# Performance work log

Hardware: AMD Instinct MI355X
Metric: run time of the kernel (lower is better)

The kernel has to match this reference:

```python
import jax, jax.numpy as jnp
import numpy as np

DIM = 192
NUM_HEADS = 6
WH, WW = 7, 7
N = WH * WW  # 49 tokens per window
C2 = 2 * DIM  # concatenated channel dim = 384
SCALE = (DIM // NUM_HEADS) ** -0.5  # module uses dim//num_heads, not C2//num_heads
NW = 64  # number of windows per image
B_ = 2048  # num_windows * batch


def _relative_position_index():
    ch = np.arange(WH)
    cw = np.arange(WW)
    coords = np.stack(np.meshgrid(ch, cw, indexing='ij')).reshape(2, -1)  # [2, N]
    rel = coords[:, :, None] - coords[:, None, :]  # [2, N, N]
    rel = rel.transpose(1, 2, 0).astype(np.int64)  # [N, N, 2]
    rel[..., 0] += WH - 1
    rel[..., 1] += WW - 1
    rel[..., 0] *= 2 * WW - 1
    return jnp.asarray(rel.sum(-1))  # [N, N]

REL_IDX = _relative_position_index()


def setup_inputs() -> dict:
    key = jax.random.key(0)
    ks = jax.random.split(key, 8)
    x = jax.random.normal(ks[0], (B_, N, DIM), dtype=jnp.float32)
    y = jax.random.normal(ks[1], (B_, N, DIM), dtype=jnp.float32)
    mask = jax.random.normal(ks[2], (NW, N, N), dtype=jnp.float32)
    w_qkv = jax.random.normal(ks[3], (6 * DIM, C2), dtype=jnp.float32) * 0.02
    b_qkv = jnp.zeros((6 * DIM,), dtype=jnp.float32)
    w_proj = jax.random.normal(ks[4], (DIM, C2), dtype=jnp.float32) * 0.02
    b_proj = jnp.zeros((DIM,), dtype=jnp.float32)
    bias_table = jax.random.normal(ks[5], ((2 * WH - 1) * (2 * WW - 1), NUM_HEADS), dtype=jnp.float32) * 0.02
    return {"x": x, "y": y, "mask": mask, "w_qkv": w_qkv, "b_qkv": b_qkv,
            "w_proj": w_proj, "b_proj": b_proj, "bias_table": bias_table}


def reference(x, y, mask, w_qkv, b_qkv, w_proj, b_proj, bias_table):
    Bc = x.shape[0]
    Dh = C2 // NUM_HEADS  # 64
    xy = jnp.concatenate([x, y], axis=2)  # [B_, N, 2*dim]
    qkv = xy @ w_qkv.T + b_qkv  # [B_, N, 6*dim]
    qkv = qkv.reshape(Bc, N, 3, NUM_HEADS, Dh).transpose(2, 0, 3, 1, 4)  # [3, B_, H, N, Dh]
    q, k, v = qkv[0] * SCALE, qkv[1], qkv[2]
    attn = jnp.einsum('bhnd,bhmd->bhnm', q, k)  # [B_, H, N, N]
    rpb = bias_table[REL_IDX]  # [N, N, H]
    attn = attn + rpb.transpose(2, 0, 1)[None]
    nW = mask.shape[0]
    attn = attn.reshape(Bc // nW, nW, NUM_HEADS, N, N) + mask[None, :, None]
    attn = attn.reshape(Bc, NUM_HEADS, N, N)
    attn = jax.nn.softmax(attn, axis=-1)
    out = jnp.einsum('bhnm,bhmd->bhnd', attn, v)  # [B_, H, N, Dh]
    out = out.transpose(0, 2, 1, 3).reshape(Bc, N, C2)
    return out @ w_proj.T + b_proj  # [B_, N, dim]
```

## Files before the change

### kernel.cpp

```cpp
#include <hip/hip_runtime.h>
#include <hip/hip_bf16.h>


typedef __attribute__((ext_vector_type(8))) short short8;
typedef __attribute__((ext_vector_type(4))) float f32x4;

#define SCALE 0.17677669529663687f

#define WQF_OFF    0ul
#define WQF_BYTES  (864ul*1024)
#define WPF_OFF    (WQF_OFF + WQF_BYTES)
#define WPF_BYTES  (144ul*1024)
#define COMB_OFF   (WPF_OFF + WPF_BYTES)
#define COMB_BYTES (64ul*6*4096*4)
#define XYF_OFF    (COMB_OFF + COMB_BYTES)
#define XYF_BYTES  (2048ul*48*1024)
#define OF_OFF     (XYF_OFF + XYF_BYTES)
#define OF_BYTES   XYF_BYTES
#define WS_NEED    (OF_OFF + OF_BYTES)

__device__ __forceinline__ unsigned short f2bf(float f){
  unsigned u = __builtin_bit_cast(unsigned, f);
  u = u + 0x7fffu + ((u >> 16) & 1u);
  return (unsigned short)(u >> 16);
}
__device__ __forceinline__ unsigned long long pack4(float4 v){
  return (unsigned long long)f2bf(v.x) | ((unsigned long long)f2bf(v.y) << 16)
       | ((unsigned long long)f2bf(v.z) << 32) | ((unsigned long long)f2bf(v.w) << 48);
}

__global__ void k0_wfrag(const float* __restrict__ wq_f, const float* __restrict__ wp_f,
                         unsigned short* __restrict__ wqf, unsigned short* __restrict__ wpf){
  int t = blockIdx.x*256 + threadIdx.x;
  int fragidx = t >> 6, l = t & 63;
  const float* src; unsigned short* dst;
  if (fragidx < 864){
    int h = fragidx/144, rem = fragidx - h*144;
    int ct = rem/12, kt = rem - ct*12;
    int row = (ct>>2)*384 + h*64 + (ct&3)*16 + (l&15);
    src = wq_f + (long)row*384 + kt*32 + (l>>4)*8;
    dst = wqf + (long)fragidx*512 + l*8;
  } else {
    int fid = fragidx - 864;
    int ct = fid/12, kt = fid - ct*12;
    int row = ct*16 + (l&15);
    src = wp_f + (long)row*384 + kt*32 + (l>>4)*8;
    dst = wpf + (long)fid*512 + l*8;
  }
  short8 v;
  #pragma unroll
  for (int e = 0; e < 8; ++e) v[e] = (short)f2bf(src[e]);
  *(short8*)dst = v;
}

__global__ void prep_comb(const float* __restrict__ mask, const float* __restrict__ btab,
                          float* __restrict__ comb){
  int idx = blockIdx.x * 256 + threadIdx.x;
  int j = idx & 63, i = (idx >> 6) & 63, rest = idx >> 12;
  int h = rest % 6, w = rest / 6;
  float v;
  if (i < 49 && j < 49){
    int di = i / 7 - j / 7 + 6;
    int dj = i % 7 - j % 7 + 6;
    v = btab[(di * 13 + dj) * 6 + h] + mask[(w * 49 + i) * 49 + j];
  } else {
    v = (j >= 49) ? -1e30f : 0.0f;
  }
  comb[idx] = v;
}

__global__ void k1_xyfrag(const float* __restrict__ x, const float* __restrict__ y,
                          unsigned short* __restrict__ xyf){
  const int kt  = blockIdx.x;
  const int win = blockIdx.y;
  const int mt  = threadIdx.x >> 6;
  const int l   = threadIdx.x & 63;
  const int row = mt*16 + (l & 15);
  const int c0  = kt*32 + (l >> 4)*8;
  short8 v = {};
  if (row < 49){
    const float* src = (kt < 6) ? (x + ((long)win*49 + row)*192 + c0)
                                : (y + ((long)win*49 + row)*192 + (c0 - 192));
    float4 f0 = *(const float4*)src, f1 = *(const float4*)(src+4);
    unsigned long long lo = pack4(f0), hi = pack4(f1);
    #pragma unroll
    for (int e = 0; e < 4; ++e){ v[e] = (short)(lo >> (16*e)); v[4+e] = (short)(hi >> (16*e)); }
  }
  *(short8*)(xyf + (((long)win*12 + kt)*4 + mt)*512 + l*8) = v;
}

__device__ __forceinline__ int swz(int r, int b){ return b ^ ((r & 7) << 4); }
__device__ __forceinline__ int a_q (int r, int c){ return 0     + swz(r, r*128 + c*2); }
__device__ __forceinline__ int a_k (int r, int c){ return 8192  + swz(r, r*128 + c*2); }
__device__ __forceinline__ int a_vt(int r, int c){ return 16384 + swz(r, r*128 + c*2); }

__global__ __launch_bounds__(256, 4)
void k2_qkv_attn(const unsigned short* __restrict__ xyf, const unsigned short* __restrict__ wqf,
                 const float* __restrict__ bqkv, const float* __restrict__ comb,
                 unsigned short* __restrict__ Of){
  __shared__ __align__(16) unsigned char smem[24576];
  const int h = blockIdx.x, win = blockIdx.y;
  const int tid = threadIdx.x, w = tid>>6, l = tid&63, l15 = l&15, lg = l>>4;

  float bias[3];
  #pragma unroll
  for (int nt = 0; nt < 3; ++nt){
    int n = w*48 + nt*16 + l15;
    bias[nt] = bqkv[(n>>6)*384 + h*64 + (n&63)];
  }

  f32x4 acc[4][3] = {};
  const unsigned short* Ab = xyf + (long)win*24576;
  const unsigned short* Bb = wqf + ((long)h*12 + w*3)*12*512;
  short8 aA[2][4], bB[2][3];
  #pragma unroll
  for (int mt = 0; mt < 4; ++mt) aA[0][mt] = *(const short8*)(Ab + mt*512 + l*8);
  #pragma unroll
  for (int nt = 0; nt < 3; ++nt) bB[0][nt] = *(const short8*)(Bb + (nt*12)*512 + l*8);
  #pragma unroll
  for (int kt = 0; kt < 12; ++kt){
    const int cur = kt & 1, nxt = cur ^ 1;
    if (kt < 11){
      #pragma unroll
      for (int mt = 0; mt < 4; ++mt)
        aA[nxt][mt] = *(const short8*)(Ab + ((kt+1)*4 + mt)*512 + l*8);
      #pragma unroll
      for (int nt = 0; nt < 3; ++nt)
        bB[nxt][nt] = *(const short8*)(Bb + (nt*12 + kt+1)*512 + l*8);
    }
    #pragma unroll
    for (int nt = 0; nt < 3; ++nt){
      #pragma unroll
      for (int mt = 0; mt < 4; ++mt)
        acc[mt][nt] = __builtin_amdgcn_mfma_f32_16x16x32_bf16(aA[cur][mt], bB[cur][nt], acc[mt][nt], 0, 0, 0);
    }
  }

  const float* cb = comb + ((long)((win & 63)*6 + h))*4096 + (w*16 + l15)*64 + lg*4;
  float4 cbv[4];
  #pragma unroll
  for (int nt = 0; nt < 4; ++nt) cbv[nt] = *(const float4*)(cb + nt*16);

  #pragma unroll
  for (int nt = 0; nt < 3; ++nt){
    int ct = w*3 + nt, s = ct >> 2, d16 = (ct & 3) * 16;
    if (s == 2){
      #pragma unroll
      for (int mt = 0; mt < 4; ++mt){
        float4 vv;
        vv.x = acc[mt][nt][0] + bias[nt]; vv.y = acc[mt][nt][1] + bias[nt];
        vv.z = acc[mt][nt][2] + bias[nt]; vv.w = acc[mt][nt][3] + bias[nt];
        *(unsigned long long*)(smem + a_vt(d16 + l15, mt*16 + lg*4)) = pack4(vv);
      }
    } else {
      float sc = (s == 0) ? SCALE : 1.0f;
      #pragma unroll
      for (int mt = 0; mt < 4; ++mt){
        #pragma unroll
        for (int j = 0; j < 4; ++j){
          int row = mt*16 + lg*4 + j;
          float v = (acc[mt][nt][j] + bias[nt]) * sc;
          int addr = (s == 0) ? a_q(row, d16 + l15) : a_k(row, d16 + l15);
          *(unsigned short*)(smem + addr) = f2bf(v);
        }
      }
    }
  }
  __syncthreads();

  short8 bq[2];
  #pragma unroll
  for (int ks = 0; ks < 2; ++ks)
    bq[ks] = *(const short8*)(smem + a_q(w*16 + l15, ks*32 + lg*8));
  f32x4 st[4] = {};
  #pragma unroll
  for (int ks = 0; ks < 2; ++ks){
    #pragma unroll
    for (int nt = 0; nt < 4; ++nt){
      short8 ak = *(const short8*)(smem + a_k(nt*16 + l15, ks*32 + lg*8));
      st[nt] = __builtin_amdgcn_mfma_f32_16x16x32_bf16(ak, bq[ks], st[nt], 0, 0, 0);
    }
  }
  #pragma unroll
  for (int nt = 0; nt < 4; ++nt){
    st[nt][0] += cbv[nt].x; st[nt][1] += cbv[nt].y;
    st[nt][2] += cbv[nt].z; st[nt][3] += cbv[nt].w;
  }
  float mx;
  {
    float m0 = fmaxf(fmaxf(st[0][0], st[0][1]), fmaxf(st[0][2], st[0][3]));
    float m1 = fmaxf(fmaxf(st[1][0], st[1][1]), fmaxf(st[1][2], st[1][3]));
    float m2 = fmaxf(fmaxf(st[2][0], st[2][1]), fmaxf(st[2][2], st[2][3]));
    float m3 = fmaxf(fmaxf(st[3][0], st[3][1]), fmaxf(st[3][2], st[3][3]));
    mx = fmaxf(fmaxf(m0, m1), fmaxf(m2, m3));
  }
  mx = fmaxf(mx, __shfl_xor(mx, 16));
  mx = fmaxf(mx, __shfl_xor(mx, 32));
  float ssum = 0.f;
  #pragma unroll
  for (int nt = 0; nt < 4; ++nt){
    #pragma unroll
    for (int j = 0; j < 4; ++j){
      float e = __expf(st[nt][j] - mx);
      st[nt][j] = e; ssum += e;
    }
  }
  ssum += __shfl_xor(ssum, 16);
  ssum += __shfl_xor(ssum, 32);
  const float inv = 1.0f / ssum;

  #pragma unroll
  for (int nt = 0; nt < 4; ++nt){
    float4 vv;
    vv.x = st[nt][0]*inv; vv.y = st[nt][1]*inv; vv.z = st[nt][2]*inv; vv.w = st[nt][3]*inv;
    *(unsigned long long*)(smem + a_q(w*16 + l15, nt*16 + lg*4)) = pack4(vv);
  }

  short8 ap[2];
  #pragma unroll
  for (int ks = 0; ks < 2; ++ks)
    ap[ks] = *(const short8*)(smem + a_q(w*16 + l15, ks*32 + lg*8));
  f32x4 oacc[4] = {};
  #pragma unroll
  for (int ks = 0; ks < 2; ++ks){
    #pragma unroll
    for (int nt = 0; nt < 4; ++nt){
      short8 bv = *(const short8*)(smem + a_vt(nt*16 + l15, ks*32 + lg*8));
      oacc[nt] = __builtin_amdgcn_mfma_f32_16x16x32_bf16(ap[ks], bv, oacc[nt], 0, 0, 0);
    }
  }
  #pragma unroll
  for (int nt = 0; nt < 4; ++nt){
    #pragma unroll
    for (int j = 0; j < 4; ++j)
      *(unsigned short*)(smem + a_q(w*16 + lg*4 + j, nt*16 + l15)) = f2bf(oacc[nt][j]);
  }
  unsigned short* Ob = Of + (((long)win*12 + h*2)*4 + w)*512 + l*8;
  #pragma unroll
  for (int ks = 0; ks < 2; ++ks){
    short8 o8 = *(const short8*)(smem + a_q(w*16 + l15, ks*32 + lg*8));
    *(short8*)(Ob + ks*4*512) = o8;
  }
}

__global__ __launch_bounds__(256, 4)
void k3_proj(const unsigned short* __restrict__ Of, const unsigned short* __restrict__ wpf,
             const float* __restrict__ bproj, float* __restrict__ out){
  const int win = blockIdx.x;
  const int tid = threadIdx.x, w = tid>>6, l = tid&63, l15 = l&15, lg = l>>4;
  float bp[3]; int np[3];
  #pragma unroll
  for (int nt = 0; nt < 3; ++nt){
    np[nt] = w*48 + nt*16 + l15;
    bp[nt] = bproj[np[nt]];
  }
  f32x4 acc[4][3] = {};
  const unsigned short* Ab = Of + (long)win*24576;
  const unsigned short* Bb = wpf + (long)(w*3)*12*512;
  short8 aA[2][4], bB[2][3];
  #pragma unroll
  for (int mt = 0; mt < 4; ++mt) aA[0][mt] = *(const short8*)(Ab + mt*512 + l*8);
  #pragma unroll
  for (int nt = 0; nt < 3; ++nt) bB[0][nt] = *(const short8*)(Bb + (nt*12)*512 + l*8);
  #pragma unroll
  for (int kt = 0; kt < 12; ++kt){
    const int cur = kt & 1, nxt = cur ^ 1;
    if (kt < 11){
      #pragma unroll
      for (int mt = 0; mt < 4; ++mt)
        aA[nxt][mt] = *(const short8*)(Ab + ((kt+1)*4 + mt)*512 + l*8);
      #pragma unroll
      for (int nt = 0; nt < 3; ++nt)
        bB[nxt][nt] = *(const short8*)(Bb + (nt*12 + kt+1)*512 + l*8);
    }
    #pragma unroll
    for (int nt = 0; nt < 3; ++nt){
      #pragma unroll
      for (int mt = 0; mt < 4; ++mt)
        acc[mt][nt] = __builtin_amdgcn_mfma_f32_16x16x32_bf16(aA[cur][mt], bB[cur][nt], acc[mt][nt], 0, 0, 0);
    }
  }
  #pragma unroll
  for (int mt = 0; mt < 4; ++mt){
    #pragma unroll
    for (int j = 0; j < 4; ++j){
      int row = mt*16 + lg*4 + j;
      if (row < 49){
        float* o = out + ((long)win*49 + row)*192;
        #pragma unroll
        for (int nt = 0; nt < 3; ++nt)
          o[np[nt]] = acc[mt][nt][j] + bp[nt];
      }
    }
  }
}

#define FB_WQ_ELEMS (1152*384)
#define FB_WP_ELEMS (192*384)
#define FB_WP_OFF   (FB_WQ_ELEMS*2)
#define FB_COMB_OFF (FB_WP_OFF + FB_WP_ELEMS*2)

__global__ void prep_weights_fb(const float* __restrict__ wq_f, const float* __restrict__ wp_f,
                                unsigned short* __restrict__ wq, unsigned short* __restrict__ wp){
  int gid = blockIdx.x * 256 + threadIdx.x;
  if (gid < FB_WQ_ELEMS) wq[gid] = f2bf(wq_f[gid]);
  else { int g = gid - FB_WQ_ELEMS; if (g < FB_WP_ELEMS) wp[g] = f2bf(wp_f[g]); }
}
__device__ __forceinline__ int fb_xy(int r, int c){ return 0      + swz(r, r*768 + c*2); }
__device__ __forceinline__ int fb_q (int r, int c){ return 49152  + swz(r, r*128 + c*2); }
__device__ __forceinline__ int fb_k (int r, int c){ return 57344  + swz(r, r*128 + c*2); }
__device__ __forceinline__ int fb_vt(int r, int c){ return 65536  + swz(r, r*128 + c*2); }
__device__ __forceinline__ int fb_p (int r, int c){ return 73728  + swz(r, r*128 + c*2); }

__global__ __launch_bounds__(256, 2)
void fused_attn_fb(const float* __restrict__ x, const float* __restrict__ y,
                   const float* __restrict__ bqkv, const float* __restrict__ bproj,
                   const unsigned short* __restrict__ wq, const unsigned short* __restrict__ wp,
                   const float* __restrict__ comb, float* __restrict__ out){
  __shared__ __align__(16) unsigned char smem[81920];
  const int b = blockIdx.x, tid = threadIdx.x;
  const int w = tid>>6, l = tid&63, l15 = l&15, lg = l>>4;
  {
    const float4* x4 = (const float4*)x + b * 2352;
    const float4* y4 = (const float4*)y + b * 2352;
    for (int idx = tid; idx < 2352; idx += 256){
      int r = idx / 48, c4 = (idx % 48) * 4;
      float4 vx = x4[idx], vy = y4[idx];
      *(unsigned long long*)(smem + fb_xy(r, c4))       = pack4(vx);
      *(unsigned long long*)(smem + fb_xy(r, 192 + c4)) = pack4(vy);
    }
    for (int idx = tid; idx < 1440; idx += 256){
      int r = 49 + idx / 96, c4 = (idx % 96) * 4;
      *(unsigned long long*)(smem + fb_xy(r, c4)) = 0ull;
    }
  }
  __syncthreads();
  const float* cbB = comb + (long)(b & 63) * (6 * 4096);
  f32x4 pacc[4][3] = {};
  int np[3]; float bp[3];
  #pragma unroll
  for (int nt = 0; nt < 3; ++nt){ np[nt] = w*48 + nt*16 + l15; bp[nt] = bproj[np[nt]]; }
  #pragma unroll 1
  for (int h = 0; h < 6; ++h){
    f32x4 acc[4][3] = {};
    int wrow[3]; float bias[3];
    #pragma unroll
    for (int nt = 0; nt < 3; ++nt){
      int n = np[nt];
      wrow[nt] = (n >> 6) * 384 + h * 64 + (n & 63);
      bias[nt] = bqkv[wrow[nt]];
    }
    #pragma unroll 4
    for (int kt = 0; kt < 12; ++kt){
      int k0 = kt * 32;
      short8 a[4];
      #pragma unroll
      for (int mt = 0; mt < 4; ++mt)
        a[mt] = *(const short8*)(smem + fb_xy(mt*16 + l15, k0 + lg*8));
      #pragma unroll
      for (int nt = 0; nt < 3; ++nt){
        short8 bb = *(const short8*)(wq + (long)wrow[nt]*384 + k0 + lg*8);
        #pragma unroll
        for (int mt = 0; mt < 4; ++mt)
          acc[mt][nt] = __builtin_amdgcn_mfma_f32_16x16x32_bf16(a[mt], bb, acc[mt][nt], 0, 0, 0);
      }
    }
    #pragma unroll
    for (int nt = 0; nt < 3; ++nt){
      int n = np[nt], s = n >> 6, d = n & 63;
      #pragma unroll
      for (int mt = 0; mt < 4; ++mt){
        #pragma unroll
        for (int j = 0; j < 4; ++j){
          int row = mt*16 + lg*4 + j;
          float v = acc[mt][nt][j] + bias[nt];
          if (s == 0) v *= SCALE;
          int addr = (s==0) ? fb_q(row,d) : (s==1) ? fb_k(row,d) : fb_vt(d,row);
          *(unsigned short*)(smem + addr) = f2bf(v);
        }
      }
    }
    __syncthreads();
    short8 aq[2];
    #pragma unroll
    for (int ks = 0; ks < 2; ++ks)
      aq[ks] = *(const short8*)(smem + fb_q(w*16 + l15, ks*32 + lg*8));
    f32x4 sacc[4] = {};
    #pragma unroll
    for (int ks = 0; ks < 2; ++ks)
      #pragma unroll
      for (int nt = 0; nt < 4; ++nt){
        short8 bk = *(const short8*)(smem + fb_k(nt*16 + l15, ks*32 + lg*8));
        sacc[nt] = __builtin_amdgcn_mfma_f32_16x16x32_bf16(aq[ks], bk, sacc[nt], 0, 0, 0);
      }
    const float* cb = cbB + h * 4096;
    float rs[4];
    #pragma unroll
    for (int j = 0; j < 4; ++j){
      int r = w*16 + lg*4 + j;
      #pragma unroll
      for (int nt = 0; nt < 4; ++nt) sacc[nt][j] += cb[r*64 + nt*16 + l15];
      float m = fmaxf(fmaxf(sacc[0][j], sacc[1][j]), fmaxf(sacc[2][j], sacc[3][j]));
      #pragma unroll
      for (int dlt = 1; dlt < 16; dlt <<= 1) m = fmaxf(m, __shfl_xor(m, dlt));
      float ssum = 0.f;
      #pragma unroll
      for (int nt = 0; nt < 4; ++nt){
        float e = __expf(sacc[nt][j] - m);
        sacc[nt][j] = e; ssum += e;
      }
      #pragma unroll
      for (int dlt = 1; dlt < 16; dlt <<= 1) ssum += __shfl_xor(ssum, dlt);
      rs[j] = ssum;
      #pragma unroll
      for (int nt = 0; nt < 4; ++nt)
        *(unsigned short*)(smem + fb_p(r, nt*16 + l15)) = f2bf(sacc[nt][j]);
    }
    short8 ap[2];
    #pragma unroll
    for (int ks = 0; ks < 2; ++ks)
      ap[ks] = *(const short8*)(smem + fb_p(w*16 + l15, ks*32 + lg*8));
    f32x4 oacc[4] = {};
    #pragma unroll
    for (int ks = 0; ks < 2; ++ks)
      #pragma unroll
      for (int nt = 0; nt < 4; ++nt){
        short8 bv = *(const short8*)(smem + fb_vt(nt*16 + l15, ks*32 + lg*8));
        oacc[nt] = __builtin_amdgcn_mfma_f32_16x16x32_bf16(ap[ks], bv, oacc[nt], 0, 0, 0);
      }
    float inv[4];
    #pragma unroll
    for (int j = 0; j < 4; ++j) inv[j] = 1.0f / rs[j];
    #pragma unroll
    for (int nt = 0; nt < 4; ++nt)
      #pragma unroll
      for (int j = 0; j < 4; ++j){
        int row = w*16 + lg*4 + j;
        *(unsigned short*)(smem + fb_p(row, nt*16 + l15)) = f2bf(oacc[nt][j] * inv[j]);
      }
    __syncthreads();
    #pragma unroll
    for (int ks = 0; ks < 2; ++ks){
      short8 ao8[4];
      #pragma unroll
      for (int mt = 0; mt < 4; ++mt)
        ao8[mt] = *(const short8*)(smem + fb_p(mt*16 + l15, ks*32 + lg*8));
      #pragma unroll
      for (int nt = 0; nt < 3; ++nt){
        short8 bb = *(const short8*)(wp + (long)np[nt]*384 + h*64 + ks*32 + lg*8);
        #pragma unroll
        for (int mt = 0; mt < 4; ++mt)
          pacc[mt][nt] = __builtin_amdgcn_mfma_f32_16x16x32_bf16(ao8[mt], bb, pacc[mt][nt], 0, 0, 0);
      }
    }
  }
  #pragma unroll
  for (int mt = 0; mt < 4; ++mt)
    #pragma unroll
    for (int j = 0; j < 4; ++j){
      int row = mt*16 + lg*4 + j;
      if (row < 49){
        float* o = out + ((long)b*49 + row)*192;
        #pragma unroll
        for (int nt = 0; nt < 3; ++nt)
          o[np[nt]] = pacc[mt][nt][j] + bp[nt];
      }
    }
}

extern "C" void kernel_launch(void* const* d_in, const int* in_sizes, int n_in,
                              void* d_out, int out_size, void* d_ws, size_t ws_size,
                              hipStream_t stream){
  (void)in_sizes; (void)n_in; (void)out_size;
  const float* x     = (const float*)d_in[0];
  const float* y     = (const float*)d_in[1];
  const float* mask  = (const float*)d_in[2];
  const float* wq_f  = (const float*)d_in[3];
  const float* bqkv  = (const float*)d_in[4];
  const float* wp_f  = (const float*)d_in[5];
  const float* bproj = (const float*)d_in[6];
  const float* btab  = (const float*)d_in[7];
  float* out = (float*)d_out;

  if (ws_size >= WS_NEED){
    unsigned short* wqf = (unsigned short*)((char*)d_ws + WQF_OFF);
    unsigned short* wpf = (unsigned short*)((char*)d_ws + WPF_OFF);
    float*          cmb = (float*)((char*)d_ws + COMB_OFF);
    unsigned short* xyf = (unsigned short*)((char*)d_ws + XYF_OFF);
    unsigned short* Ofr = (unsigned short*)((char*)d_ws + OF_OFF);
    hipLaunchKernelGGL(k0_wfrag,    dim3(252),     dim3(256), 0, stream, wq_f, wp_f, wqf, wpf);
    hipLaunchKernelGGL(prep_comb,   dim3(6144),    dim3(256), 0, stream, mask, btab, cmb);
    hipLaunchKernelGGL(k1_xyfrag,   dim3(12,2048), dim3(256), 0, stream, x, y, xyf);
    hipLaunchKernelGGL(k2_qkv_attn, dim3(6,2048),  dim3(256), 0, stream, xyf, wqf, bqkv, cmb, Ofr);
    hipLaunchKernelGGL(k3_proj,     dim3(2048),    dim3(256), 0, stream, Ofr, wpf, bproj, out);
  } else {
    unsigned short* wq  = (unsigned short*)d_ws;
    unsigned short* wp  = (unsigned short*)((char*)d_ws + FB_WP_OFF);
    float*          cmb = (float*)((char*)d_ws + FB_COMB_OFF);
    hipLaunchKernelGGL(prep_weights_fb, dim3(2016), dim3(256), 0, stream, wq_f, wp_f, wq, wp);
    hipLaunchKernelGGL(prep_comb,       dim3(6144), dim3(256), 0, stream, mask, btab, cmb);
    hipLaunchKernelGGL(fused_attn_fb,   dim3(2048), dim3(256), 0, stream,
                       x, y, bqkv, bproj, wq, wp, cmb, out);
  }
}
```

Baseline: 269.0 us.

## Fold scale into weights, bias into accumulators, use hardware bf16 convert and setprio

Pre-scales the Q rows of the packed QKV weight by the attention scale and initializes the MFMA accumulators with the bias, removing per-element add and multiply work in the epilogues. It replaces the software round-to-nearest bf16 conversion with the v_cvt_pk_bf16_f32 instruction. It also adds sched_barrier and s_setprio around the MFMA blocks and lowers launch_bounds occupancy from 4 to 3 to give the compiler more registers. The changes are several unrelated micro-optimizations, and the lower occupancy could reduce latency hiding.

```diff
diff --git a/kernel.cpp b/kernel.cpp
--- a/kernel.cpp
+++ b/kernel.cpp
@@ -29,17 +29,31 @@
        | ((unsigned long long)f2bf(v.z) << 32) | ((unsigned long long)f2bf(v.w) << 48);
 }
 
+__device__ __forceinline__ unsigned short cvt1(float x){
+  unsigned r;
+  asm("v_cvt_pk_bf16_f32 %0, %1, %1" : "=v"(r) : "v"(x));
+  return (unsigned short)r;
+}
+__device__ __forceinline__ uint2 pk4(float a, float b, float c, float d){
+  unsigned lo, hi;
+  asm("v_cvt_pk_bf16_f32 %0, %1, %2" : "=v"(lo) : "v"(a), "v"(b));
+  asm("v_cvt_pk_bf16_f32 %0, %1, %2" : "=v"(hi) : "v"(c), "v"(d));
+  return make_uint2(lo, hi);
+}
+
 __global__ void k0_wfrag(const float* __restrict__ wq_f, const float* __restrict__ wp_f,
                          unsigned short* __restrict__ wqf, unsigned short* __restrict__ wpf){
   int t = blockIdx.x*256 + threadIdx.x;
   int fragidx = t >> 6, l = t & 63;
   const float* src; unsigned short* dst;
+  float sc = 1.0f;
   if (fragidx < 864){
     int h = fragidx/144, rem = fragidx - h*144;
     int ct = rem/12, kt = rem - ct*12;
     int row = (ct>>2)*384 + h*64 + (ct&3)*16 + (l&15);
     src = wq_f + (long)row*384 + kt*32 + (l>>4)*8;
     dst = wqf + (long)fragidx*512 + l*8;
+    if (ct < 4) sc = SCALE;
   } else {
     int fid = fragidx - 864;
     int ct = fid/12, kt = fid - ct*12;
@@ -49,7 +63,7 @@
   }
   short8 v;
   #pragma unroll
-  for (int e = 0; e < 8; ++e) v[e] = (short)f2bf(src[e]);
+  for (int e = 0; e < 8; ++e) v[e] = (short)f2bf(src[e] * sc);
   *(short8*)dst = v;
 }
 
@@ -94,7 +108,7 @@
 __device__ __forceinline__ int a_k (int r, int c){ return 8192  + swz(r, r*128 + c*2); }
 __device__ __forceinline__ int a_vt(int r, int c){ return 16384 + swz(r, r*128 + c*2); }
 
-__global__ __launch_bounds__(256, 4)
+__global__ __launch_bounds__(256, 3)
 void k2_qkv_attn(const unsigned short* __restrict__ xyf, const unsigned short* __restrict__ wqf,
                  const float* __restrict__ bqkv, const float* __restrict__ comb,
                  unsigned short* __restrict__ Of){
@@ -105,11 +119,11 @@
   float bias[3];
   #pragma unroll
   for (int nt = 0; nt < 3; ++nt){
-    int n = w*48 + nt*16 + l15;
-    bias[nt] = bqkv[(n>>6)*384 + h*64 + (n&63)];
-  }
-
-  f32x4 acc[4][3] = {};
+    int ct = w*3 + nt, s = ct >> 2;
+    bias[nt] = bqkv[s*384 + h*64 + (ct & 3)*16 + l15];
+    if (s == 0) bias[nt] *= SCALE;
+  }
+
   const unsigned short* Ab = xyf + (long)win*24576;
   const unsigned short* Bb = wqf + ((long)h*12 + w*3)*12*512;
   short8 aA[2][4], bB[2][3];
@@ -117,6 +131,15 @@
   for (int mt = 0; mt < 4; ++mt) aA[0][mt] = *(const short8*)(Ab + mt*512 + l*8);
   #pragma unroll
   for (int nt = 0; nt < 3; ++nt) bB[0][nt] = *(const short8*)(Bb + (nt*12)*512 + l*8);
+
+  f32x4 acc[4][3];
+  #pragma unroll
+  for (int mt = 0; mt < 4; ++mt)
+    #pragma unroll
+    for (int nt = 0; nt < 3; ++nt)
+      #pragma unroll
+      for (int j = 0; j < 4; ++j) acc[mt][nt][j] = bias[nt];
+
   #pragma unroll
   for (int kt = 0; kt < 12; ++kt){
     const int cur = kt & 1, nxt = cur ^ 1;
@@ -128,12 +151,15 @@
       for (int nt = 0; nt < 3; ++nt)
         bB[nxt][nt] = *(const short8*)(Bb + (nt*12 + kt+1)*512 + l*8);
     }
+    __builtin_amdgcn_sched_barrier(0);
+    __builtin_amdgcn_s_setprio(1);
     #pragma unroll
     for (int nt = 0; nt < 3; ++nt){
       #pragma unroll
       for (int mt = 0; mt < 4; ++mt)
         acc[mt][nt] = __builtin_amdgcn_mfma_f32_16x16x32_bf16(aA[cur][mt], bB[cur][nt], acc[mt][nt], 0, 0, 0);
     }
+    __builtin_amdgcn_s_setprio(0);
   }
 
   const float* cb = comb + ((long)((win & 63)*6 + h))*4096 + (w*16 + l15)*64 + lg*4;
@@ -147,21 +173,17 @@
     if (s == 2){
       #pragma unroll
       for (int mt = 0; mt < 4; ++mt){
-        float4 vv;
-        vv.x = acc[mt][nt][0] + bias[nt]; vv.y = acc[mt][nt][1] + bias[nt];
-        vv.z = acc[mt][nt][2] + bias[nt]; vv.w = acc[mt][nt][3] + bias[nt];
-        *(unsigned long long*)(smem + a_vt(d16 + l15, mt*16 + lg*4)) = pack4(vv);
+        uint2 p = pk4(acc[mt][nt][0], acc[mt][nt][1], acc[mt][nt][2], acc[mt][nt][3]);
+        *(uint2*)(smem + a_vt(d16 + l15, mt*16 + lg*4)) = p;
       }
     } else {
-      float sc = (s == 0) ? SCALE : 1.0f;
       #pragma unroll
       for (int mt = 0; mt < 4; ++mt){
         #pragma unroll
         for (int j = 0; j < 4; ++j){
           int row = mt*16 + lg*4 + j;
-          float v = (acc[mt][nt][j] + bias[nt]) * sc;
           int addr = (s == 0) ? a_q(row, d16 + l15) : a_k(row, d16 + l15);
-          *(unsigned short*)(smem + addr) = f2bf(v);
+          *(unsigned short*)(smem + addr) = cvt1(acc[mt][nt][j]);
         }
       }
     }
@@ -173,6 +195,7 @@
   for (int ks = 0; ks < 2; ++ks)
     bq[ks] = *(const short8*)(smem + a_q(w*16 + l15, ks*32 + lg*8));
   f32x4 st[4] = {};
+  __builtin_amdgcn_s_setprio(1);
   #pragma unroll
   for (int ks = 0; ks < 2; ++ks){
     #pragma unroll
@@ -181,6 +204,7 @@
       st[nt] = __builtin_amdgcn_mfma_f32_16x16x32_bf16(ak, bq[ks], st[nt], 0, 0, 0);
     }
   }
+  __builtin_amdgcn_s_setprio(0);
   #pragma unroll
   for (int nt = 0; nt < 4; ++nt){
     st[nt][0] += cbv[nt].x; st[nt][1] += cbv[nt].y;
@@ -211,9 +235,8 @@
 
   #pragma unroll
   for (int nt = 0; nt < 4; ++nt){
-    float4 vv;
-    vv.x = st[nt][0]*inv; vv.y = st[nt][1]*inv; vv.z = st[nt][2]*inv; vv.w = st[nt][3]*inv;
-    *(unsigned long long*)(smem + a_q(w*16 + l15, nt*16 + lg*4)) = pack4(vv);
+    uint2 p = pk4(st[nt][0]*inv, st[nt][1]*inv, st[nt][2]*inv, st[nt][3]*inv);
+    *(uint2*)(smem + a_q(w*16 + l15, nt*16 + lg*4)) = p;
   }
 
   short8 ap[2];
@@ -221,6 +244,7 @@
   for (int ks = 0; ks < 2; ++ks)
     ap[ks] = *(const short8*)(smem + a_q(w*16 + l15, ks*32 + lg*8));
   f32x4 oacc[4] = {};
+  __builtin_amdgcn_s_setprio(1);
   #pragma unroll
   for (int ks = 0; ks < 2; ++ks){
     #pragma unroll
@@ -229,11 +253,12 @@
       oacc[nt] = __builtin_amdgcn_mfma_f32_16x16x32_bf16(ap[ks], bv, oacc[nt], 0, 0, 0);
     }
   }
+  __builtin_amdgcn_s_setprio(0);
   #pragma unroll
   for (int nt = 0; nt < 4; ++nt){
     #pragma unroll
     for (int j = 0; j < 4; ++j)
-      *(unsigned short*)(smem + a_q(w*16 + lg*4 + j, nt*16 + l15)) = f2bf(oacc[nt][j]);
+      *(unsigned short*)(smem + a_q(w*16 + lg*4 + j, nt*16 + l15)) = cvt1(oacc[nt][j]);
   }
   unsigned short* Ob = Of + (((long)win*12 + h*2)*4 + w)*512 + l*8;
   #pragma unroll
@@ -243,7 +268,7 @@
   }
 }
 
-__global__ __launch_bounds__(256, 4)
+__global__ __launch_bounds__(256, 3)
 void k3_proj(const unsigned short* __restrict__ Of, const unsigned short* __restrict__ wpf,
              const float* __restrict__ bproj, float* __restrict__ out){
   const int win = blockIdx.x;
@@ -254,7 +279,6 @@
     np[nt] = w*48 + nt*16 + l15;
     bp[nt] = bproj[np[nt]];
   }
-  f32x4 acc[4][3] = {};
   const unsigned short* Ab = Of + (long)win*24576;
   const unsigned short* Bb = wpf + (long)(w*3)*12*512;
   short8 aA[2][4], bB[2][3];
@@ -262,6 +286,13 @@
   for (int mt = 0; mt < 4; ++mt) aA[0][mt] = *(const short8*)(Ab + mt*512 + l*8);
   #pragma unroll
   for (int nt = 0; nt < 3; ++nt) bB[0][nt] = *(const short8*)(Bb + (nt*12)*512 + l*8);
+  f32x4 acc[4][3];
+  #pragma unroll
+  for (int mt = 0; mt < 4; ++mt)
+    #pragma unroll
+    for (int nt = 0; nt < 3; ++nt)
+      #pragma unroll
+      for (int j = 0; j < 4; ++j) acc[mt][nt][j] = bp[nt];
   #pragma unroll
   for (int kt = 0; kt < 12; ++kt){
     const int cur = kt & 1, nxt = cur ^ 1;
@@ -273,12 +304,15 @@
       for (int nt = 0; nt < 3; ++nt)
         bB[nxt][nt] = *(const short8*)(Bb + (nt*12 + kt+1)*512 + l*8);
     }
+    __builtin_amdgcn_sched_barrier(0);
+    __builtin_amdgcn_s_setprio(1);
     #pragma unroll
     for (int nt = 0; nt < 3; ++nt){
       #pragma unroll
       for (int mt = 0; mt < 4; ++mt)
         acc[mt][nt] = __builtin_amdgcn_mfma_f32_16x16x32_bf16(aA[cur][mt], bB[cur][nt], acc[mt][nt], 0, 0, 0);
     }
+    __builtin_amdgcn_s_setprio(0);
   }
   #pragma unroll
   for (int mt = 0; mt < 4; ++mt){
@@ -289,7 +323,7 @@
         float* o = out + ((long)win*49 + row)*192;
         #pragma unroll
         for (int nt = 0; nt < 3; ++nt)
-          o[np[nt]] = acc[mt][nt][j] + bp[nt];
+          o[np[nt]] = acc[mt][nt][j];
       }
     }
   }
```

After: 251.6 us. 6.5% less time.
